# Kernel optimization log

Measured on AMD Instinct MI355X. Metric: run time of the kernel, lower is better.

The kernel has to match this reference:

```python
import jax, jax.numpy as jnp
import numpy as np

B, S, D = 2, 2048, 2048
H = 16
NOPE, ROPE, VDIM = 128, 64, 128
QKD = NOPE + ROPE  # 192
KV_RANK = 512
EPS = 1e-6
SCALE = QKD ** -0.5  # rope_factor <= 1.0 -> no mscale correction


def _rotate_half(x):
    h = x.shape[-1] // 2
    return jnp.concatenate([-x[..., h:], x[..., :h]], axis=-1)


def _rms_norm(x, w):
    var = jnp.mean(jnp.square(x), axis=-1, keepdims=True)
    return x * jax.lax.rsqrt(var + EPS) * w


def setup_inputs() -> dict:
    key = jax.random.key(0)
    ks = jax.random.split(key, 8)
    hidden_states = jax.random.normal(ks[0], (B, S, D), dtype=jnp.float32)
    cos = jax.random.uniform(ks[1], (S, ROPE), dtype=jnp.float32)
    sin = jax.random.uniform(ks[2], (S, ROPE), dtype=jnp.float32)
    # parameters (torch Linear stores [out, in]; keep same layout)
    wq_w = jax.random.normal(ks[3], (H * QKD, D), dtype=jnp.float32) * (D ** -0.5)
    wkv_a_w = jax.random.normal(ks[4], (KV_RANK + ROPE, D), dtype=jnp.float32) * (D ** -0.5)
    kv_norm_w = jnp.ones((KV_RANK,), dtype=jnp.float32)
    wkv_b_w = jax.random.normal(ks[5], (H * (NOPE + VDIM), KV_RANK), dtype=jnp.float32) * (KV_RANK ** -0.5)
    wo_w = jax.random.normal(ks[6], (D, H * VDIM), dtype=jnp.float32) * ((H * VDIM) ** -0.5)
    return dict(hidden_states=hidden_states, cos=cos, sin=sin,
                wq_w=wq_w, wkv_a_w=wkv_a_w, kv_norm_w=kv_norm_w,
                wkv_b_w=wkv_b_w, wo_w=wo_w)


def reference(hidden_states, cos, sin, wq_w, wkv_a_w, kv_norm_w, wkv_b_w, wo_w):
    x = hidden_states
    # q projection (q_lora_rank == 0 path)
    q = jnp.einsum('bsd,od->bso', x, wq_w).reshape(B, S, H, QKD)
    q_nope, q_pe = q[..., :NOPE], q[..., NOPE:]
    # low-rank kv
    kv_all = jnp.einsum('bsd,od->bso', x, wkv_a_w)  # [B,S,KV_RANK+ROPE]
    kv, k_pe = kv_all[..., :KV_RANK], kv_all[..., KV_RANK:]
    kv_proj = jnp.einsum('bsr,or->bso', _rms_norm(kv, kv_norm_w), wkv_b_w)
    kv_proj = kv_proj.reshape(B, S, H, NOPE + VDIM)
    k_nope, v = kv_proj[..., :NOPE], kv_proj[..., NOPE:]
    # rotary on pe parts; k_pe broadcast over heads
    c = cos[None, :, None, :]  # [1,S,1,ROPE]
    s = sin[None, :, None, :]
    q_pe = q_pe * c + _rotate_half(q_pe) * s
    k_pe_h = k_pe[:, :, None, :]  # broadcast over heads
    k_pe_h = k_pe_h * c + _rotate_half(k_pe_h) * s
    k_pe_h = jnp.broadcast_to(k_pe_h, (B, S, H, ROPE))
    k = jnp.concatenate([k_nope, k_pe_h], axis=-1)  # [B,S,H,QKD]
    qf = jnp.concatenate([q_nope, q_pe], axis=-1)
    # naive attention, fp32 softmax
    scores = jnp.einsum('bshd,bthd->bsht', qf, k) * SCALE
    attn = jax.nn.softmax(scores.astype(jnp.float32), axis=-1).astype(x.dtype)
    out = jnp.einsum('bsht,bthd->bshd', attn, v).reshape(B, S, H * VDIM)
    return jnp.einsum('bsf,of->bso', out, wo_w)
```

## Files before the change

kernel.cpp:

```cpp
#include <hip/hip_runtime.h>
#include <cstdint>


typedef _Float16 f16;
typedef _Float16 f16x8 __attribute__((ext_vector_type(8)));
typedef _Float16 f16x4 __attribute__((ext_vector_type(4)));
typedef float    f32x4 __attribute__((ext_vector_type(4)));

#define SCALE 0.07216878364870322f

__device__ __forceinline__ void gl2lds16(const void* g, void* lds_wave_base) {
  __builtin_amdgcn_global_load_lds(
      (const __attribute__((address_space(1))) uint32_t*)(uintptr_t)g,
      (__attribute__((address_space(3))) uint32_t*)(uint32_t)(uintptr_t)lds_wave_base,
      16, 0, 0);
}

__global__ __launch_bounds__(256) void k_cvt(
    const float* __restrict__ x, const float* __restrict__ wq,
    const float* __restrict__ wkvb, const float* __restrict__ wo,
    f16* __restrict__ xb, f16* __restrict__ wqb,
    f16* __restrict__ wkvbb, f16* __restrict__ wob)
{
  size_t i = ((size_t)blockIdx.x * 256 + threadIdx.x) * 4;
  const float* src; f16* dst; size_t off; float scl = 1.0f;
  if (i < 8388608ull)            { src = x;    dst = xb;    off = i; }
  else if (i < 14680064ull)      { src = wq;   dst = wqb;   off = i - 8388608ull; scl = SCALE; }
  else if (i < 16777216ull)      { src = wkvb; dst = wkvbb; off = i - 14680064ull; }
  else                           { src = wo;   dst = wob;   off = i - 16777216ull; }
  float4 v = *(const float4*)(src + off);
  f16x4 h; h[0]=(f16)(v.x*scl); h[1]=(f16)(v.y*scl); h[2]=(f16)(v.z*scl); h[3]=(f16)(v.w*scl);
  *(f16x4*)(dst + off) = h;
}

__global__ __launch_bounds__(256) void k_cvt_pad(const float* __restrict__ w,
                                                 f16* __restrict__ out)
{
  int i = (blockIdx.x * 256 + threadIdx.x) * 4;
  int r = i >> 11;
  f16x4 h;
  if (r < 576) {
    float4 v = *(const float4*)(w + i);
    h[0]=(f16)v.x; h[1]=(f16)v.y; h[2]=(f16)v.z; h[3]=(f16)v.w;
  } else { h[0]=h[1]=h[2]=h[3]=(f16)0.f; }
  *(f16x4*)(out + i) = h;
}

template<class Epi>
__device__ __forceinline__ void gemm_core(const f16* __restrict__ Ablk,
                                          const f16* __restrict__ Bblk,
                                          int K, Epi epi)
{
  __shared__ __align__(16) f16 As[128 * 64];
  __shared__ __align__(16) f16 Bs[128 * 64];

  const int tid  = threadIdx.x;
  const int lane = tid & 63;
  const int wv   = tid >> 6;
  const int wm = (wv >> 1) * 64, wn = (wv & 1) * 64;
  const int lrow = lane & 15;
  const int lk   = lane >> 4;

  f32x4 acc[4][4];
#pragma unroll
  for (int i = 0; i < 4; ++i)
#pragma unroll
    for (int j = 0; j < 4; ++j) acc[i][j] = f32x4{0.f, 0.f, 0.f, 0.f};

  for (int k0 = 0; k0 < K; k0 += 64) {
    __syncthreads();
#pragma unroll
    for (int it = 0; it < 4; ++it) {
      int s  = it * 256 + tid;
      int r  = s >> 3, sc = s & 7;
      int gc = sc ^ (r & 7);
      gl2lds16(Ablk + (size_t)r * K + k0 + gc * 8, (f16*)As + (size_t)(it * 256 + wv * 64) * 8);
      gl2lds16(Bblk + (size_t)r * K + k0 + gc * 8, (f16*)Bs + (size_t)(it * 256 + wv * 64) * 8);
    }
    __syncthreads();

#pragma unroll
    for (int ks = 0; ks < 2; ++ks) {
      f16x8 af[4], bf[4];
#pragma unroll
      for (int i = 0; i < 4; ++i) {
        int ra = wm + i * 16 + lrow;
        int ca = (ks * 4 + lk) ^ (ra & 7);
        af[i] = *(const f16x8*)(As + ra * 64 + ca * 8);
        int rb = wn + i * 16 + lrow;
        int cb = (ks * 4 + lk) ^ (rb & 7);
        bf[i] = *(const f16x8*)(Bs + rb * 64 + cb * 8);
      }
#pragma unroll
      for (int i = 0; i < 4; ++i)
#pragma unroll
        for (int j = 0; j < 4; ++j)
          acc[i][j] = __builtin_amdgcn_mfma_f32_16x16x32_f16(af[i], bf[j], acc[i][j], 0, 0, 0);
    }
  }
  epi(acc, wm, wn, lk, lrow);
}

__global__ __launch_bounds__(256, 3) void k_gemm_qkva(
    const f16* __restrict__ xb, const f16* __restrict__ wqb,
    const f16* __restrict__ wkvab, f16* __restrict__ qraw, f16* __restrict__ kva)
{
  int nb = blockIdx.x, m0 = blockIdx.y * 128;
  const f16* Bblk; f16* Cb; int ldc;
  if (nb < 24) { Bblk = wqb + (size_t)nb * 128 * 2048;
                 Cb = qraw + (size_t)m0 * 3072 + nb * 128; ldc = 3072; }
  else         { int n0 = (nb - 24) * 128;
                 Bblk = wkvab + (size_t)n0 * 2048;
                 Cb = kva + (size_t)m0 * 640 + n0; ldc = 640; }
  gemm_core(xb + (size_t)m0 * 2048, Bblk, 2048,
    [&](f32x4 (&acc)[4][4], int wm, int wn, int lk, int lrow) {
#pragma unroll
      for (int i = 0; i < 4; ++i)
#pragma unroll
        for (int rr = 0; rr < 4; ++rr) {
          int row = wm + i * 16 + lk * 4 + rr;
#pragma unroll
          for (int j = 0; j < 4; ++j)
            Cb[(size_t)row * ldc + wn + j * 16 + lrow] = (f16)acc[i][j][rr];
        }
    });
}

__global__ __launch_bounds__(256, 3) void k_gemm_kvb(
    const f16* __restrict__ kvn, const f16* __restrict__ wkvbb,
    f16* __restrict__ knope, f16* __restrict__ vf)
{
  int nb = blockIdx.x, m0 = blockIdx.y * 128;
  int hh = nb >> 1;
  bool isv = nb & 1;
  gemm_core(kvn + (size_t)m0 * 512, wkvbb + (size_t)nb * 128 * 512, 512,
    [&](f32x4 (&acc)[4][4], int wm, int wn, int lk, int lrow) {
      if (isv) {
#pragma unroll
        for (int i = 0; i < 4; ++i)
#pragma unroll
          for (int j = 0; j < 4; ++j) {
            int vd = wn + j * 16 + lrow;
            int trow = m0 + wm + i * 16 + lk * 4;
            int bb = trow >> 11, ss = trow & 2047;
            f16x4 pk;
#pragma unroll
            for (int rr = 0; rr < 4; ++rr) pk[rr] = (f16)acc[i][j][rr];
            *(f16x4*)(vf + ((size_t)(bb * 16 + hh) * 128 + vd) * 2048 + ss) = pk;
          }
      } else {
#pragma unroll
        for (int i = 0; i < 4; ++i)
#pragma unroll
          for (int rr = 0; rr < 4; ++rr) {
            int trow = m0 + wm + i * 16 + lk * 4 + rr;
#pragma unroll
            for (int j = 0; j < 4; ++j)
              knope[(size_t)trow * 2048 + hh * 128 + wn + j * 16 + lrow] = (f16)acc[i][j][rr];
          }
      }
    });
}

__global__ __launch_bounds__(256, 3) void k_gemm_out(
    const f16* __restrict__ aout, const f16* __restrict__ wob, float* __restrict__ out)
{
  int n0 = blockIdx.x * 128, m0 = blockIdx.y * 128;
  gemm_core(aout + (size_t)m0 * 2048, wob + (size_t)n0 * 2048, 2048,
    [&](f32x4 (&acc)[4][4], int wm, int wn, int lk, int lrow) {
#pragma unroll
      for (int i = 0; i < 4; ++i)
#pragma unroll
        for (int rr = 0; rr < 4; ++rr) {
          int row = m0 + wm + i * 16 + lk * 4 + rr;
#pragma unroll
          for (int j = 0; j < 4; ++j)
            out[(size_t)row * 2048 + n0 + wn + j * 16 + lrow] = acc[i][j][rr];
        }
    });
}

__global__ __launch_bounds__(256) void k_rmsnorm_rope(
    const f16* __restrict__ kva, const float* __restrict__ w,
    const float* __restrict__ cosb, const float* __restrict__ sinb,
    f16* __restrict__ kvn, f16* __restrict__ kper)
{
  int row = blockIdx.x;
  int s = row & 2047;
  const f16* in = kva + (size_t)row * 640;
  int t = threadIdx.x;
  float v0 = (float)in[t], v1 = (float)in[t + 256];
  float ss = v0 * v0 + v1 * v1;
#pragma unroll
  for (int m = 1; m < 64; m <<= 1) ss += __shfl_xor(ss, m);
  __shared__ float red[4];
  if ((t & 63) == 0) red[t >> 6] = ss;
  __syncthreads();
  float tot = red[0] + red[1] + red[2] + red[3];
  float sc = rsqrtf(tot * (1.0f / 512.0f) + 1e-6f);
  kvn[(size_t)row * 512 + t]       = (f16)(v0 * sc * w[t]);
  kvn[(size_t)row * 512 + t + 256] = (f16)(v1 * sc * w[t + 256]);
  if (t < 32) {
    float a = (float)in[512 + t], bq = (float)in[512 + t + 32];
    float c0 = cosb[s * 64 + t], s0 = sinb[s * 64 + t];
    float c1 = cosb[s * 64 + t + 32], s1 = sinb[s * 64 + t + 32];
    kper[(size_t)row * 64 + t]      = (f16)(a * c0 - bq * s0);
    kper[(size_t)row * 64 + t + 32] = (f16)(bq * c1 + a * s1);
  }
}

__global__ __launch_bounds__(256) void k_rope_q(
    f16* __restrict__ qraw, const float* __restrict__ cosb, const float* __restrict__ sinb)
{
  int idx = blockIdx.x * 256 + threadIdx.x;
  int j = idx & 31;
  int hh = (idx >> 5) & 15;
  int t = idx >> 9;
  int s = t & 2047;
  f16* base = qraw + (size_t)t * 3072 + hh * 192 + 128;
  float a = (float)base[j], bq = (float)base[j + 32];
  float c0 = cosb[s * 64 + j], s0 = sinb[s * 64 + j];
  float c1 = cosb[s * 64 + j + 32], s1 = sinb[s * 64 + j + 32];
  base[j]      = (f16)(a * c0 - bq * s0);
  base[j + 32] = (f16)(bq * c1 + a * s1);
}

#define PSTR 84

__global__ __launch_bounds__(512, 2) void k_attn(
    const f16* __restrict__ qraw, const f16* __restrict__ knope,
    const f16* __restrict__ kper, const f16* __restrict__ vf,
    f16* __restrict__ aout)
{
  int qt = blockIdx.x, h = blockIdx.y, b = blockIdx.z;
  int q0 = qt * 256;
  int tid = threadIdx.x, lane = tid & 63, wv = tid >> 6;
  int lrow = lane & 15, lk = lane >> 4;

  __shared__ __align__(16) f16 Ks[2][64 * 192];
  __shared__ __align__(16) f16 Vs[2][128 * 64];
  __shared__ __align__(16) f16 Ps[8][32 * PSTR];

  f16x8 qfr[2][6];
#pragma unroll
  for (int m = 0; m < 2; ++m) {
    const f16* qb = qraw + ((size_t)(b * 2048 + q0 + wv * 32 + m * 16 + lrow)) * 3072
                    + h * 192 + lk * 8;
#pragma unroll
    for (int ks = 0; ks < 6; ++ks) qfr[m][ks] = *(const f16x8*)(qb + ks * 32);
  }

  f32x4 oacc[2][8];
#pragma unroll
  for (int m = 0; m < 2; ++m)
#pragma unroll
    for (int i = 0; i < 8; ++i) oacc[m][i] = f32x4{0.f, 0.f, 0.f, 0.f};
  float l_st[2][4];
#pragma unroll
  for (int m = 0; m < 2; ++m)
#pragma unroll
    for (int r = 0; r < 4; ++r) l_st[m][r] = 0.f;

  const f16* knb = knope + ((size_t)b * 2048) * 2048 + h * 128;
  const f16* kpb = kper + (size_t)b * 2048 * 64;
  const f16* vb_ = vf + ((size_t)(b * 16 + h)) * 128 * 2048;

  const char* kp_ptr[3]; int kp_step[3];
#pragma unroll
  for (int it = 0; it < 3; ++it) {
    int s = it * 512 + tid;
    int r = s / 24, c = s - r * 24;
    int gc = c ^ (r & 7);
    if (gc < 16) { kp_ptr[it] = (const char*)(knb + (size_t)r * 2048 + gc * 8); kp_step[it] = 64 * 2048 * 2; }
    else         { kp_ptr[it] = (const char*)(kpb + (size_t)r * 64 + (gc - 16) * 8); kp_step[it] = 64 * 64 * 2; }
  }
  const char* vp_ptr[2];
#pragma unroll
  for (int it = 0; it < 2; ++it) {
    int s = it * 512 + tid;
    int r = s >> 3, c = s & 7, gc = c ^ (r & 7);
    vp_ptr[it] = (const char*)(vb_ + (size_t)r * 2048 + gc * 8);
  }

#pragma unroll
  for (int it = 0; it < 3; ++it) {
    gl2lds16(kp_ptr[it], (f16*)Ks[0] + (size_t)(it * 512 + wv * 64) * 8);
    kp_ptr[it] += kp_step[it];
  }
#pragma unroll
  for (int it = 0; it < 2; ++it) {
    gl2lds16(vp_ptr[it], (f16*)Vs[0] + (size_t)(it * 512 + wv * 64) * 8);
    vp_ptr[it] += 64 * 2;
  }

  int cur = 0;
  for (int t0 = 0; t0 < 2048; t0 += 64) {
    __syncthreads();
    if (t0 + 64 < 2048) {
#pragma unroll
      for (int it = 0; it < 3; ++it) {
        gl2lds16(kp_ptr[it], (f16*)Ks[cur ^ 1] + (size_t)(it * 512 + wv * 64) * 8);
        kp_ptr[it] += kp_step[it];
      }
#pragma unroll
      for (int it = 0; it < 2; ++it) {
        gl2lds16(vp_ptr[it], (f16*)Vs[cur ^ 1] + (size_t)(it * 512 + wv * 64) * 8);
        vp_ptr[it] += 64 * 2;
      }
    }
    const f16* Kc = Ks[cur];
    const f16* Vc = Vs[cur];

    f32x4 sacc[2][4];
#pragma unroll
    for (int m = 0; m < 2; ++m)
#pragma unroll
      for (int nt = 0; nt < 4; ++nt) sacc[m][nt] = f32x4{0.f, 0.f, 0.f, 0.f};
#pragma unroll
    for (int nt = 0; nt < 4; ++nt) {
      int rb = nt * 16 + lrow;
#pragma unroll
      for (int ks = 0; ks < 6; ++ks) {
        int cc = (ks * 4 + lk) ^ (rb & 7);
        f16x8 bfr = *(const f16x8*)(Kc + rb * 192 + cc * 8);
        sacc[0][nt] = __builtin_amdgcn_mfma_f32_16x16x32_f16(qfr[0][ks], bfr, sacc[0][nt], 0, 0, 0);
        sacc[1][nt] = __builtin_amdgcn_mfma_f32_16x16x32_f16(qfr[1][ks], bfr, sacc[1][nt], 0, 0, 0);
      }
    }

#pragma unroll
    for (int m = 0; m < 2; ++m) {
#pragma unroll
      for (int r = 0; r < 4; ++r) {
        float p0 = __expf(sacc[m][0][r]);
        float p1 = __expf(sacc[m][1][r]);
        float p2 = __expf(sacc[m][2][r]);
        float p3 = __expf(sacc[m][3][r]);
        l_st[m][r] += (p0 + p1) + (p2 + p3);
        int prow = (m * 16 + lk * 4 + r) * PSTR;
        Ps[wv][prow + 0 * 16 + lrow] = (f16)p0;
        Ps[wv][prow + 1 * 16 + lrow] = (f16)p1;
        Ps[wv][prow + 2 * 16 + lrow] = (f16)p2;
        Ps[wv][prow + 3 * 16 + lrow] = (f16)p3;
      }
    }
    __builtin_amdgcn_s_waitcnt(0xC07F);

#pragma unroll
    for (int ks2 = 0; ks2 < 2; ++ks2) {
      f16x8 pa0 = *(const f16x8*)(&Ps[wv][(0 * 16 + lrow) * PSTR + ks2 * 32 + lk * 8]);
      f16x8 pa1 = *(const f16x8*)(&Ps[wv][(1 * 16 + lrow) * PSTR + ks2 * 32 + lk * 8]);
#pragma unroll
      for (int nv = 0; nv < 8; ++nv) {
        int rv = nv * 16 + lrow;
        int cc = (ks2 * 4 + lk) ^ (rv & 7);
        f16x8 vbf = *(const f16x8*)(Vc + rv * 64 + cc * 8);
        oacc[0][nv] = __builtin_amdgcn_mfma_f32_16x16x32_f16(pa0, vbf, oacc[0][nv], 0, 0, 0);
        oacc[1][nv] = __builtin_amdgcn_mfma_f32_16x16x32_f16(pa1, vbf, oacc[1][nv], 0, 0, 0);
      }
    }
    cur ^= 1;
  }

  float rinv[2][4];
#pragma unroll
  for (int m = 0; m < 2; ++m)
#pragma unroll
    for (int r = 0; r < 4; ++r) {
      float l = l_st[m][r];
#pragma unroll
      for (int msk = 1; msk < 16; msk <<= 1) l += __shfl_xor(l, msk);
      rinv[m][r] = 1.0f / l;
    }
#pragma unroll
  for (int m = 0; m < 2; ++m) {
    f16* ob = aout + ((size_t)(b * 2048 + q0 + wv * 32 + m * 16 + lk * 4)) * 2048
              + h * 128 + lrow;
#pragma unroll
    for (int nv = 0; nv < 8; ++nv)
#pragma unroll
      for (int rr = 0; rr < 4; ++rr)
        ob[(size_t)rr * 2048 + nv * 16] = (f16)(oacc[m][nv][rr] * rinv[m][rr]);
  }
}

extern "C" void kernel_launch(void* const* d_in, const int* in_sizes, int n_in,
                              void* d_out, int out_size, void* d_ws, size_t ws_size,
                              hipStream_t stream)
{
  const float* x    = (const float*)d_in[0];
  const float* cosb = (const float*)d_in[1];
  const float* sinb = (const float*)d_in[2];
  const float* wq   = (const float*)d_in[3];
  const float* wkva = (const float*)d_in[4];
  const float* knw  = (const float*)d_in[5];
  const float* wkvb = (const float*)d_in[6];
  const float* wo   = (const float*)d_in[7];
  float* out = (float*)d_out;

  char* p = (char*)d_ws;
  auto take = [&](size_t elems) { char* r = p; p += (elems * 2 + 255) & ~(size_t)255; return r; };
  f16* xb    = (f16*)take(8388608ull);
  f16* wqb   = (f16*)take(6291456ull);
  f16* wkvab = (f16*)take(1310720ull);
  f16* wkvbb = (f16*)take(2097152ull);
  f16* wob   = (f16*)take(4194304ull);
  f16* qraw  = (f16*)take(12582912ull);
  f16* kva   = (f16*)take(2621440ull);
  f16* kvn   = (f16*)take(2097152ull);
  f16* kper  = (f16*)take(262144ull);
  f16* knope = (f16*)take(8388608ull);
  f16* vf    = (f16*)take(8388608ull);
  f16* aout  = (f16*)take(8388608ull);

  k_cvt<<<20480, 256, 0, stream>>>(x, wq, wkvb, wo, xb, wqb, wkvbb, wob);
  k_cvt_pad<<<1280, 256, 0, stream>>>(wkva, wkvab);
  k_gemm_qkva<<<dim3(29, 32), 256, 0, stream>>>(xb, wqb, wkvab, qraw, kva);
  k_rmsnorm_rope<<<4096, 256, 0, stream>>>(kva, knw, cosb, sinb, kvn, kper);
  k_rope_q<<<8192, 256, 0, stream>>>(qraw, cosb, sinb);
  k_gemm_kvb<<<dim3(32, 32), 256, 0, stream>>>(kvn, wkvbb, knope, vf);
  k_attn<<<dim3(8, 16, 2), 512, 0, stream>>>(qraw, knope, kper, vf, aout);
  k_gemm_out<<<dim3(16, 32), 256, 0, stream>>>(aout, wob, out);
}
```

Before: 394.9 us.

## Split attention over key halves with merge kernel and single-buffered LDS

The attention kernel now splits the 2048-key range into two halves. This doubles the grid to 512 blocks, and each block writes an unnormalized partial output plus row sums. A new merge kernel adds the two partials and normalizes them. The K/V double buffer is replaced by a single buffer with an extra barrier, and the launch bound is raised to 4 blocks per CU to increase occupancy, at the cost of losing load/compute overlap within a block. The change also shifts exponents by a constant to keep fp16 P values and partials in range, reorders the LDS K fragment loads ahead of the MFMAs, and folds the padded wkv_a conversion into the main convert kernel, which removes one launch.

```diff
diff --git a/kernel.cpp b/kernel.cpp
--- a/kernel.cpp
+++ b/kernel.cpp
@@ -19,10 +19,22 @@
 __global__ __launch_bounds__(256) void k_cvt(
     const float* __restrict__ x, const float* __restrict__ wq,
     const float* __restrict__ wkvb, const float* __restrict__ wo,
+    const float* __restrict__ wkva,
     f16* __restrict__ xb, f16* __restrict__ wqb,
-    f16* __restrict__ wkvbb, f16* __restrict__ wob)
+    f16* __restrict__ wkvbb, f16* __restrict__ wob, f16* __restrict__ wkvab)
 {
   size_t i = ((size_t)blockIdx.x * 256 + threadIdx.x) * 4;
+  if (i >= 20971520ull) {
+    size_t j = i - 20971520ull;
+    int r = (int)(j >> 11);
+    f16x4 h;
+    if (r < 576) {
+      float4 v = *(const float4*)(wkva + j);
+      h[0]=(f16)v.x; h[1]=(f16)v.y; h[2]=(f16)v.z; h[3]=(f16)v.w;
+    } else { h[0]=h[1]=h[2]=h[3]=(f16)0.f; }
+    *(f16x4*)(wkvab + j) = h;
+    return;
+  }
   const float* src; f16* dst; size_t off; float scl = 1.0f;
   if (i < 8388608ull)            { src = x;    dst = xb;    off = i; }
   else if (i < 14680064ull)      { src = wq;   dst = wqb;   off = i - 8388608ull; scl = SCALE; }
@@ -31,19 +43,6 @@
   float4 v = *(const float4*)(src + off);
   f16x4 h; h[0]=(f16)(v.x*scl); h[1]=(f16)(v.y*scl); h[2]=(f16)(v.z*scl); h[3]=(f16)(v.w*scl);
   *(f16x4*)(dst + off) = h;
-}
-
-__global__ __launch_bounds__(256) void k_cvt_pad(const float* __restrict__ w,
-                                                 f16* __restrict__ out)
-{
-  int i = (blockIdx.x * 256 + threadIdx.x) * 4;
-  int r = i >> 11;
-  f16x4 h;
-  if (r < 576) {
-    float4 v = *(const float4*)(w + i);
-    h[0]=(f16)v.x; h[1]=(f16)v.y; h[2]=(f16)v.z; h[3]=(f16)v.w;
-  } else { h[0]=h[1]=h[2]=h[3]=(f16)0.f; }
-  *(f16x4*)(out + i) = h;
 }
 
 template<class Epi>
@@ -225,20 +224,23 @@
   base[j + 32] = (f16)(bq * c1 + a * s1);
 }
 
-#define PSTR 84
-
-__global__ __launch_bounds__(512, 2) void k_attn(
+#define PSTR 76
+#define ESHIFT 8.0f
+
+__global__ __launch_bounds__(512, 4) void k_attn(
     const f16* __restrict__ qraw, const f16* __restrict__ knope,
     const f16* __restrict__ kper, const f16* __restrict__ vf,
-    f16* __restrict__ aout)
-{
-  int qt = blockIdx.x, h = blockIdx.y, b = blockIdx.z;
+    f16* __restrict__ opart, float* __restrict__ lpart)
+{
+  int qt = blockIdx.x & 7, sp = blockIdx.x >> 3;
+  int h = blockIdx.y, b = blockIdx.z;
   int q0 = qt * 256;
+  int tb = sp * 1024;
   int tid = threadIdx.x, lane = tid & 63, wv = tid >> 6;
   int lrow = lane & 15, lk = lane >> 4;
 
-  __shared__ __align__(16) f16 Ks[2][64 * 192];
-  __shared__ __align__(16) f16 Vs[2][128 * 64];
+  __shared__ __align__(16) f16 Ks[64 * 192];
+  __shared__ __align__(16) f16 Vs[128 * 64];
   __shared__ __align__(16) f16 Ps[8][32 * PSTR];
 
   f16x8 qfr[2][6];
@@ -261,9 +263,9 @@
 #pragma unroll
     for (int r = 0; r < 4; ++r) l_st[m][r] = 0.f;
 
-  const f16* knb = knope + ((size_t)b * 2048) * 2048 + h * 128;
-  const f16* kpb = kper + (size_t)b * 2048 * 64;
-  const f16* vb_ = vf + ((size_t)(b * 16 + h)) * 128 * 2048;
+  const f16* knb = knope + ((size_t)(b * 2048 + tb)) * 2048 + h * 128;
+  const f16* kpb = kper + (size_t)(b * 2048 + tb) * 64;
+  const f16* vb_ = vf + ((size_t)(b * 16 + h)) * 128 * 2048 + tb;
 
   const char* kp_ptr[3]; int kp_step[3];
 #pragma unroll
@@ -282,34 +284,19 @@
     vp_ptr[it] = (const char*)(vb_ + (size_t)r * 2048 + gc * 8);
   }
 
-#pragma unroll
-  for (int it = 0; it < 3; ++it) {
-    gl2lds16(kp_ptr[it], (f16*)Ks[0] + (size_t)(it * 512 + wv * 64) * 8);
-    kp_ptr[it] += kp_step[it];
-  }
-#pragma unroll
-  for (int it = 0; it < 2; ++it) {
-    gl2lds16(vp_ptr[it], (f16*)Vs[0] + (size_t)(it * 512 + wv * 64) * 8);
-    vp_ptr[it] += 64 * 2;
-  }
-
-  int cur = 0;
-  for (int t0 = 0; t0 < 2048; t0 += 64) {
+  for (int t0 = 0; t0 < 1024; t0 += 64) {
     __syncthreads();
-    if (t0 + 64 < 2048) {
-#pragma unroll
-      for (int it = 0; it < 3; ++it) {
-        gl2lds16(kp_ptr[it], (f16*)Ks[cur ^ 1] + (size_t)(it * 512 + wv * 64) * 8);
-        kp_ptr[it] += kp_step[it];
-      }
-#pragma unroll
-      for (int it = 0; it < 2; ++it) {
-        gl2lds16(vp_ptr[it], (f16*)Vs[cur ^ 1] + (size_t)(it * 512 + wv * 64) * 8);
-        vp_ptr[it] += 64 * 2;
-      }
-    }
-    const f16* Kc = Ks[cur];
-    const f16* Vc = Vs[cur];
+#pragma unroll
+    for (int it = 0; it < 3; ++it) {
+      gl2lds16(kp_ptr[it], (f16*)Ks + (size_t)(it * 512 + wv * 64) * 8);
+      kp_ptr[it] += kp_step[it];
+    }
+#pragma unroll
+    for (int it = 0; it < 2; ++it) {
+      gl2lds16(vp_ptr[it], (f16*)Vs + (size_t)(it * 512 + wv * 64) * 8);
+      vp_ptr[it] += 64 * 2;
+    }
+    __syncthreads();
 
     f32x4 sacc[2][4];
 #pragma unroll
@@ -317,14 +304,18 @@
 #pragma unroll
       for (int nt = 0; nt < 4; ++nt) sacc[m][nt] = f32x4{0.f, 0.f, 0.f, 0.f};
 #pragma unroll
-    for (int nt = 0; nt < 4; ++nt) {
-      int rb = nt * 16 + lrow;
-#pragma unroll
-      for (int ks = 0; ks < 6; ++ks) {
+    for (int ks = 0; ks < 6; ++ks) {
+      f16x8 bfr[4];
+#pragma unroll
+      for (int nt = 0; nt < 4; ++nt) {
+        int rb = nt * 16 + lrow;
         int cc = (ks * 4 + lk) ^ (rb & 7);
-        f16x8 bfr = *(const f16x8*)(Kc + rb * 192 + cc * 8);
-        sacc[0][nt] = __builtin_amdgcn_mfma_f32_16x16x32_f16(qfr[0][ks], bfr, sacc[0][nt], 0, 0, 0);
-        sacc[1][nt] = __builtin_amdgcn_mfma_f32_16x16x32_f16(qfr[1][ks], bfr, sacc[1][nt], 0, 0, 0);
+        bfr[nt] = *(const f16x8*)(Ks + rb * 192 + cc * 8);
+      }
+#pragma unroll
+      for (int nt = 0; nt < 4; ++nt) {
+        sacc[0][nt] = __builtin_amdgcn_mfma_f32_16x16x32_f16(qfr[0][ks], bfr[nt], sacc[0][nt], 0, 0, 0);
+        sacc[1][nt] = __builtin_amdgcn_mfma_f32_16x16x32_f16(qfr[1][ks], bfr[nt], sacc[1][nt], 0, 0, 0);
       }
     }
 
@@ -332,10 +323,10 @@
     for (int m = 0; m < 2; ++m) {
 #pragma unroll
       for (int r = 0; r < 4; ++r) {
-        float p0 = __expf(sacc[m][0][r]);
-        float p1 = __expf(sacc[m][1][r]);
-        float p2 = __expf(sacc[m][2][r]);
-        float p3 = __expf(sacc[m][3][r]);
+        float p0 = __expf(sacc[m][0][r] - ESHIFT);
+        float p1 = __expf(sacc[m][1][r] - ESHIFT);
+        float p2 = __expf(sacc[m][2][r] - ESHIFT);
+        float p3 = __expf(sacc[m][3][r] - ESHIFT);
         l_st[m][r] += (p0 + p1) + (p2 + p3);
         int prow = (m * 16 + lk * 4 + r) * PSTR;
         Ps[wv][prow + 0 * 16 + lrow] = (f16)p0;
@@ -354,15 +345,13 @@
       for (int nv = 0; nv < 8; ++nv) {
         int rv = nv * 16 + lrow;
         int cc = (ks2 * 4 + lk) ^ (rv & 7);
-        f16x8 vbf = *(const f16x8*)(Vc + rv * 64 + cc * 8);
+        f16x8 vbf = *(const f16x8*)(Vs + rv * 64 + cc * 8);
         oacc[0][nv] = __builtin_amdgcn_mfma_f32_16x16x32_f16(pa0, vbf, oacc[0][nv], 0, 0, 0);
         oacc[1][nv] = __builtin_amdgcn_mfma_f32_16x16x32_f16(pa1, vbf, oacc[1][nv], 0, 0, 0);
       }
     }
-    cur ^= 1;
-  }
-
-  float rinv[2][4];
+  }
+
 #pragma unroll
   for (int m = 0; m < 2; ++m)
 #pragma unroll
@@ -370,18 +359,40 @@
       float l = l_st[m][r];
 #pragma unroll
       for (int msk = 1; msk < 16; msk <<= 1) l += __shfl_xor(l, msk);
-      rinv[m][r] = 1.0f / l;
+      if (lrow == 0) {
+        int row = q0 + wv * 32 + m * 16 + lk * 4 + r;
+        lpart[((size_t)((sp * 2 + b) * 2048 + row)) * 16 + h] = l;
+      }
     }
 #pragma unroll
   for (int m = 0; m < 2; ++m) {
-    f16* ob = aout + ((size_t)(b * 2048 + q0 + wv * 32 + m * 16 + lk * 4)) * 2048
+    f16* ob = opart + ((size_t)((sp * 2 + b) * 2048 + q0 + wv * 32 + m * 16 + lk * 4)) * 2048
               + h * 128 + lrow;
 #pragma unroll
     for (int nv = 0; nv < 8; ++nv)
 #pragma unroll
       for (int rr = 0; rr < 4; ++rr)
-        ob[(size_t)rr * 2048 + nv * 16] = (f16)(oacc[m][nv][rr] * rinv[m][rr]);
-  }
+        ob[(size_t)rr * 2048 + nv * 16] = (f16)oacc[m][nv][rr];
+  }
+}
+
+__global__ __launch_bounds__(256) void k_merge(
+    const f16* __restrict__ opart, const float* __restrict__ lpart,
+    f16* __restrict__ aout)
+{
+  int t = blockIdx.x;
+  int b = t >> 11, s = t & 2047;
+  int col = threadIdx.x * 8;
+  int h = col >> 7;
+  float l0 = lpart[((size_t)(b * 2048 + s)) * 16 + h];
+  float l1 = lpart[((size_t)((2 + b) * 2048 + s)) * 16 + h];
+  float rinv = 1.0f / (l0 + l1);
+  f16x8 o0 = *(const f16x8*)(opart + ((size_t)(b * 2048 + s)) * 2048 + col);
+  f16x8 o1 = *(const f16x8*)(opart + ((size_t)((2 + b) * 2048 + s)) * 2048 + col);
+  f16x8 o;
+#pragma unroll
+  for (int k = 0; k < 8; ++k) o[k] = (f16)(((float)o0[k] + (float)o1[k]) * rinv);
+  *(f16x8*)(aout + (size_t)t * 2048 + col) = o;
 }
 
 extern "C" void kernel_launch(void* const* d_in, const int* in_sizes, int n_in,
@@ -412,13 +423,15 @@
   f16* knope = (f16*)take(8388608ull);
   f16* vf    = (f16*)take(8388608ull);
   f16* aout  = (f16*)take(8388608ull);
-
-  k_cvt<<<20480, 256, 0, stream>>>(x, wq, wkvb, wo, xb, wqb, wkvbb, wob);
-  k_cvt_pad<<<1280, 256, 0, stream>>>(wkva, wkvab);
+  f16* opart = (f16*)take(16777216ull);
+  float* lpart = (float*)take(262144ull);
+
+  k_cvt<<<21760, 256, 0, stream>>>(x, wq, wkvb, wo, wkva, xb, wqb, wkvbb, wob, wkvab);
   k_gemm_qkva<<<dim3(29, 32), 256, 0, stream>>>(xb, wqb, wkvab, qraw, kva);
   k_rmsnorm_rope<<<4096, 256, 0, stream>>>(kva, knw, cosb, sinb, kvn, kper);
   k_rope_q<<<8192, 256, 0, stream>>>(qraw, cosb, sinb);
   k_gemm_kvb<<<dim3(32, 32), 256, 0, stream>>>(kvn, wkvbb, knope, vf);
-  k_attn<<<dim3(8, 16, 2), 512, 0, stream>>>(qraw, knope, kper, vf, aout);
+  k_attn<<<dim3(16, 16, 2), 512, 0, stream>>>(qraw, knope, kper, vf, opart, lpart);
+  k_merge<<<4096, 256, 0, stream>>>(opart, lpart, aout);
   k_gemm_out<<<dim3(16, 32), 256, 0, stream>>>(aout, wob, out);
 }
```

After: 651.9 us. 1.65x slower.
